# Kernel tuning notes

Hardware: AMD Instinct MI355X
Metric: run time of the kernel (lower is better)

The kernel has to match this reference:

```python
import jax, jax.numpy as jnp
import numpy as np

B, N, DIM, HEADS, DH, EDGE, DEPTH, K = 4, 128, 256, 8, 64, 64, 2, 512
INNER = HEADS * DH
SCALE = DH ** -0.5


def _ln(x, g, b, eps=1e-5):
    m = x.mean(-1, keepdims=True)
    v = ((x - m) ** 2).mean(-1, keepdims=True)
    return (x - m) / jnp.sqrt(v + eps) * g + b


def _rotate_half(x):
    # interleaved pairs: (d r) with r=2 -> (-x2, x1)
    xp = x.reshape(x.shape[:-1] + (-1, 2))
    x1, x2 = xp[..., 0], xp[..., 1]
    return jnp.stack((-x2, x1), axis=-1).reshape(x.shape)


def _gated_res(x, res, gw):
    gate = jax.nn.sigmoid(jnp.concatenate((x, res, x - res), axis=-1) @ gw)
    return x * gate + res * (1 - gate)


def forward(nodes, edges, edge_ln_g, edge_ln_b, ln1_g, ln1_b, w_exp, b_exp,
            w_q, b_q, w_kv, b_kv, w_ekv, b_ekv, w_out, b_out, gate1_w,
            ln2_g, ln2_b, w_ff1, b_ff1, w_ff2, b_ff2, gate2_w, codebook):
    b, n = nodes.shape[:2]
    # LayerNorm edges over channel dim: (B,C,N,N) -> (B,N,N,C)
    e = _ln(jnp.transpose(edges, (0, 2, 3, 1)), edge_ln_g, edge_ln_b)
    # rotary frequencies over positions, repeated pairwise -> (1, N, DH)
    inv = 1.0 / (10000.0 ** (jnp.arange(0, DH, 2, dtype=jnp.float32) / DH))
    fr = jnp.repeat(jnp.arange(n, dtype=jnp.float32)[:, None] * inv[None, :], 2, axis=-1)
    cos, sin = jnp.cos(fr)[None], jnp.sin(fr)[None]

    def heads3(t):  # (B,N,H*D) -> (B*H,N,D)
        return t.reshape(b, n, HEADS, DH).transpose(0, 2, 1, 3).reshape(b * HEADS, n, DH)

    for i in range(DEPTH):
        # PreNorm + edge-conditioned attention
        x = _ln(nodes, ln1_g[i], ln1_b[i])
        x = x @ w_exp[i] + b_exp[i]
        q = x @ w_q[i] + b_q[i]
        k, v = jnp.split(x @ w_kv[i] + b_kv[i], 2, axis=-1)
        ekv = e @ w_ekv[i] + b_ekv[i]  # (B,N,N,INNER)
        q, k, v = heads3(q), heads3(k), heads3(v)
        ekv = ekv.reshape(b, n, n, HEADS, DH).transpose(0, 3, 1, 2, 4).reshape(b * HEADS, n, n, DH)
        q = q * cos + _rotate_half(q) * sin
        k = k * cos + _rotate_half(k) * sin
        kk = k[:, None, :, :] + ekv  # (BH, i, j, d)
        vv = v[:, None, :, :] + ekv
        sim = jnp.einsum('bid,bijd->bij', q, kk) * SCALE
        att = jax.nn.softmax(sim, axis=-1)
        out = jnp.einsum('bij,bijd->bid', att, vv)
        out = out.reshape(b, HEADS, n, DH).transpose(0, 2, 1, 3).reshape(b, n, INNER)
        out = out @ w_out[i] + b_out[i]
        nodes = _gated_res(out, nodes, gate1_w[i])
        # PreNorm + FeedForward
        h = _ln(nodes, ln2_g[i], ln2_b[i])
        h = jax.nn.gelu(h @ w_ff1[i] + b_ff1[i], approximate=False) @ w_ff2[i] + b_ff2[i]
        nodes = _gated_res(h, nodes, gate2_w[i])

    # VQ codebook nearest-neighbor lookup with straight-through estimator
    z = nodes.reshape(-1, DIM)
    d = (z * z).sum(-1, keepdims=True) - 2.0 * z @ codebook.T + (codebook * codebook).sum(-1)[None, :]
    idx = jnp.argmin(d, axis=-1)
    zq = codebook[idx].reshape(b, n, DIM)
    return nodes + jax.lax.stop_gradient(zq - nodes)


def setup_inputs() -> dict:
    key = jax.random.key(0)
    ks = jax.random.split(key, 16)
    s = 0.02
    inp = {
        'nodes': jax.random.normal(ks[0], (B, N, DIM), jnp.float32),
        'edges': jax.random.normal(ks[1], (B, EDGE, N, N), jnp.float32),
        'edge_ln_g': jnp.ones((EDGE,), jnp.float32),
        'edge_ln_b': jnp.zeros((EDGE,), jnp.float32),
        'ln1_g': jnp.ones((DEPTH, DIM), jnp.float32),
        'ln1_b': jnp.zeros((DEPTH, DIM), jnp.float32),
        'w_exp': s * jax.random.normal(ks[2], (DEPTH, DIM, INNER), jnp.float32),
        'b_exp': jnp.zeros((DEPTH, INNER), jnp.float32),
        'w_q': s * jax.random.normal(ks[3], (DEPTH, INNER, INNER), jnp.float32),
        'b_q': jnp.zeros((DEPTH, INNER), jnp.float32),
        'w_kv': s * jax.random.normal(ks[4], (DEPTH, INNER, 2 * INNER), jnp.float32),
        'b_kv': jnp.zeros((DEPTH, 2 * INNER), jnp.float32),
        'w_ekv': s * jax.random.normal(ks[5], (DEPTH, EDGE, INNER), jnp.float32),
        'b_ekv': jnp.zeros((DEPTH, INNER), jnp.float32),
        'w_out': s * jax.random.normal(ks[6], (DEPTH, INNER, DIM), jnp.float32),
        'b_out': jnp.zeros((DEPTH, DIM), jnp.float32),
        'gate1_w': s * jax.random.normal(ks[7], (DEPTH, 3 * DIM, 1), jnp.float32),
        'ln2_g': jnp.ones((DEPTH, DIM), jnp.float32),
        'ln2_b': jnp.zeros((DEPTH, DIM), jnp.float32),
        'w_ff1': s * jax.random.normal(ks[8], (DEPTH, DIM, 4 * DIM), jnp.float32),
        'b_ff1': jnp.zeros((DEPTH, 4 * DIM), jnp.float32),
        'w_ff2': s * jax.random.normal(ks[9], (DEPTH, 4 * DIM, DIM), jnp.float32),
        'b_ff2': jnp.zeros((DEPTH, DIM), jnp.float32),
        'gate2_w': s * jax.random.normal(ks[10], (DEPTH, 3 * DIM, 1), jnp.float32),
        'codebook': jax.random.uniform(ks[11], (K, DIM), jnp.float32, -1.0 / K, 1.0 / K),
    }
    return inp


def reference(nodes, edges, edge_ln_g, edge_ln_b, ln1_g, ln1_b, w_exp, b_exp,
              w_q, b_q, w_kv, b_kv, w_ekv, b_ekv, w_out, b_out, gate1_w,
              ln2_g, ln2_b, w_ff1, b_ff1, w_ff2, b_ff2, gate2_w, codebook):
    return forward(nodes, edges, edge_ln_g, edge_ln_b, ln1_g, ln1_b, w_exp, b_exp,
                   w_q, b_q, w_kv, b_kv, w_ekv, b_ekv, w_out, b_out, gate1_w,
                   ln2_g, ln2_b, w_ff1, b_ff1, w_ff2, b_ff2, gate2_w, codebook)
```

## Files before the change

kernel.cpp:

```cpp
#include <hip/hip_runtime.h>
#include <math.h>


#define DEV __device__ __forceinline__

constexpr int Bn = 4, Nn = 128, DIMn = 256, HEADSn = 8, DHn = 64, EDGEn = 64,
              DEPTHn = 2, Kn = 512, INNERn = 512;
constexpr int QKVW = 1536;
constexpr int PART = 131072;

DEV float wave_reduce_sum(float v) {
#pragma unroll
  for (int m = 32; m >= 1; m >>= 1) v += __shfl_xor(v, m);
  return v;
}

DEV float block_reduce_sum_256(float v, float* red) {
  v = wave_reduce_sum(v);
  int tid = threadIdx.x;
  if ((tid & 63) == 0) red[tid >> 6] = v;
  __syncthreads();
  v = red[0] + red[1] + red[2] + red[3];
  __syncthreads();
  return v;
}

DEV float gelu_exact(float x) {
  return 0.5f * x * (1.f + erff(x * 0.70710678118654752f));
}

__global__ __launch_bounds__(256) void prep_kernel(
    const float* __restrict__ edges, const float* __restrict__ eg,
    const float* __restrict__ eb, float* __restrict__ e,
    float* __restrict__ eT, float* __restrict__ cost, float* __restrict__ sint,
    const float* __restrict__ nodes_in, const float* __restrict__ ln1_g,
    const float* __restrict__ ln1_b, float* __restrict__ xln,
    float* __restrict__ nodes, const float* __restrict__ wek,
    const float* __restrict__ w_out, const float* __restrict__ bek,
    const float* __restrict__ b_out, float* __restrict__ W2,
    float* __restrict__ b_out2, const float* __restrict__ w_exp,
    const float* __restrict__ b_exp, const float* __restrict__ w_q,
    const float* __restrict__ b_q, const float* __restrict__ w_kv,
    const float* __restrict__ b_kv, float* __restrict__ WqkvF,
    float* __restrict__ bqkvF) {
  __shared__ __align__(16) float smem[4736];
  int blk = blockIdx.x;
  int tid = threadIdx.x;

  if (blk < 12) {
    int t = blk;
    int l = t / 6, seg = t % 6;
    int n = seg * 256 + tid;
    const float* W;
    int ldw;
    float acc;
    if (n < 512) {
      W = w_q + (size_t)l * 512 * 512 + n;
      ldw = 512;
      acc = b_q[l * 512 + n];
    } else {
      W = w_kv + (size_t)l * 512 * 1024 + (n - 512);
      ldw = 1024;
      acc = b_kv[l * 1024 + (n - 512)];
    }
    const float* be = b_exp + l * 512;
#pragma unroll 8
    for (int k = 0; k < 512; ++k) acc += be[k] * W[(size_t)k * ldw];
    bqkvF[l * 1536 + n] = acc;
  } else if (blk < 396) {
    int t = blk - 12;
    int l = t / 192, r = t % 192;
    int by = r / 24, bx = r % 24;
    float* As = smem;
    float* Bs = smem + 32 * 34;
    int n0 = bx * 64;
    const float* Aab = w_exp + (size_t)l * 256 * 512 + (size_t)(by * 32) * 512;
    const float* Wb;
    int ldw;
    if (n0 < 512) {
      Wb = w_q + (size_t)l * 512 * 512 + n0;
      ldw = 512;
    } else {
      Wb = w_kv + (size_t)l * 512 * 1024 + (n0 - 512);
      ldw = 1024;
    }
    int arow = tid >> 3, acol = (tid & 7) << 2;
    int brow = tid >> 4, bcol = (tid & 15) << 2;
    int tx = tid & 15, ty = tid >> 4;
    float4 a_nxt = *(const float4*)(Aab + (size_t)arow * 512 + acol);
    float4 b0_nxt = *(const float4*)(Wb + (size_t)brow * ldw + bcol);
    float4 b1_nxt = *(const float4*)(Wb + (size_t)(brow + 16) * ldw + bcol);
    float acc[2][4] = {};
    for (int k0 = 0; k0 < 512; k0 += 32) {
      As[(acol + 0) * 34 + arow] = a_nxt.x;
      As[(acol + 1) * 34 + arow] = a_nxt.y;
      As[(acol + 2) * 34 + arow] = a_nxt.z;
      As[(acol + 3) * 34 + arow] = a_nxt.w;
      *(float4*)&Bs[brow * 68 + bcol] = b0_nxt;
      *(float4*)&Bs[(brow + 16) * 68 + bcol] = b1_nxt;
      __syncthreads();
      int kn = k0 + 32;
      if (kn < 512) {
        a_nxt = *(const float4*)(Aab + (size_t)arow * 512 + kn + acol);
        b0_nxt = *(const float4*)(Wb + (size_t)(kn + brow) * ldw + bcol);
        b1_nxt = *(const float4*)(Wb + (size_t)(kn + brow + 16) * ldw + bcol);
      }
#pragma unroll
      for (int kk = 0; kk < 32; ++kk) {
        float2 av = *(const float2*)&As[kk * 34 + ty * 2];
        float4 bv = *(const float4*)&Bs[kk * 68 + tx * 4];
        acc[0][0] += av.x * bv.x;
        acc[0][1] += av.x * bv.y;
        acc[0][2] += av.x * bv.z;
        acc[0][3] += av.x * bv.w;
        acc[1][0] += av.y * bv.x;
        acc[1][1] += av.y * bv.y;
        acc[1][2] += av.y * bv.z;
        acc[1][3] += av.y * bv.w;
      }
      __syncthreads();
    }
#pragma unroll
    for (int u = 0; u < 2; ++u) {
      int d = by * 32 + ty * 2 + u;
      float4 o = {acc[u][0], acc[u][1], acc[u][2], acc[u][3]};
      *(float4*)(WqkvF + (size_t)l * 256 * 1536 + (size_t)d * 1536 + n0 +
                 tx * 4) = o;
    }
  } else if (blk < 908) {
    float* ets = smem;
    float* redS = smem + 4224;
    float* redQ = smem + 4480;
    int eidx = blk - 396;
    int i = eidx & 127, b = eidx >> 7;
    int j = tid & 127, half = tid >> 7;
    const float* src = edges + (size_t)b * EDGEn * Nn * Nn +
                       (size_t)(half * 32) * (Nn * Nn) + i * Nn + j;
    float vals[32];
    float s = 0.f, q = 0.f;
#pragma unroll
    for (int cc = 0; cc < 32; ++cc) {
      float x = src[(size_t)cc * (Nn * Nn)];
      vals[cc] = x;
      s += x;
      q += x * x;
    }
    redS[tid] = s;
    redQ[tid] = q;
    __syncthreads();
    float ts = redS[j] + redS[j + 128];
    float tq = redQ[j] + redQ[j + 128];
    float m = ts * (1.0f / 64.0f);
    float var = tq * (1.0f / 64.0f) - m * m;
    float inv = 1.f / sqrtf(var + 1e-5f);
    float* dst = e + ((size_t)(b * Nn + i) * EDGEn) * Nn + j;
#pragma unroll
    for (int cc = 0; cc < 32; ++cc) {
      int c = half * 32 + cc;
      float o = (vals[cc] - m) * inv * eg[c] + eb[c];
      vals[cc] = o;
      dst[(size_t)c * Nn] = o;
    }
    float* dstT = eT + ((size_t)(b * Nn + i) * Nn) * EDGEn;
#pragma unroll
    for (int ch = 0; ch < 2; ++ch) {
      __syncthreads();
      if (half == ch) {
#pragma unroll
        for (int cc = 0; cc < 32; ++cc) ets[j * 33 + cc] = vals[cc];
      }
      __syncthreads();
#pragma unroll
      for (int it = 0; it < 4; ++it) {
        int f4 = it * 256 + tid;
        int jj = f4 >> 3, c4 = (f4 & 7) << 2;
        float4 o4 = {ets[jj * 33 + c4], ets[jj * 33 + c4 + 1],
                     ets[jj * 33 + c4 + 2], ets[jj * 33 + c4 + 3]};
        *(float4*)(dstT + (size_t)jj * EDGEn + ch * 32 + c4) = o4;
      }
    }
  } else if (blk < 972) {
    int t = blk - 908;
    int l = t >> 5, h = (t >> 2) & 7, nt = t & 3;
    float* As = smem;
    float* Bs = smem + 2304;
    const float* wekl = wek + (size_t)l * 64 * 512 + h * 64;
    const float* woutl =
        w_out + (size_t)l * 512 * 256 + (size_t)(h * 64) * 256 + nt * 64;
    int tx = tid & 15, ty = tid >> 4;
    float acc[4][4] = {};
    for (int d0 = 0; d0 < 64; d0 += 32) {
      for (int f = tid; f < 512; f += 256) {
        int c = f >> 3, d4 = (f & 7) << 2;
        *(float4*)&As[c * 36 + d4] =
            *(const float4*)(wekl + (size_t)c * 512 + d0 + d4);
      }
      for (int f = tid; f < 512; f += 256) {
        int dd = f >> 4, n4 = (f & 15) << 2;
        *(float4*)&Bs[dd * 68 + n4] =
            *(const float4*)(woutl + (size_t)(d0 + dd) * 256 + n4);
      }
      __syncthreads();
#pragma unroll
      for (int dd = 0; dd < 32; ++dd) {
        float4 bv = *(const float4*)&Bs[dd * 68 + tx * 4];
#pragma unroll
        for (int u = 0; u < 4; ++u) {
          float a = As[(ty * 4 + u) * 36 + dd];
          acc[u][0] += a * bv.x;
          acc[u][1] += a * bv.y;
          acc[u][2] += a * bv.z;
          acc[u][3] += a * bv.w;
        }
      }
      __syncthreads();
    }
#pragma unroll
    for (int u = 0; u < 4; ++u) {
      float4 o = {acc[u][0], acc[u][1], acc[u][2], acc[u][3]};
      *(float4*)(W2 + (size_t)l * 512 * 256 +
                 (size_t)(h * 64 + ty * 4 + u) * 256 + nt * 64 + tx * 4) = o;
    }
  } else if (blk < 980) {
    int t = blk - 972;
    int l = t >> 2, nt = t & 3;
    float* part = smem;
    int nn = tid & 63, kq = tid >> 6;
    const float* wcol = w_out + (size_t)l * 512 * 256 + nt * 64 + nn;
    float acc = 0.f;
    for (int k = kq * 128; k < kq * 128 + 128; ++k)
      acc += bek[l * 512 + k] * wcol[(size_t)k * 256];
    part[tid] = acc;
    __syncthreads();
    if (tid < 64)
      b_out2[l * 256 + nt * 64 + nn] =
          b_out[l * 256 + nt * 64 + nn] + part[nn] + part[64 + nn] +
          part[128 + nn] + part[192 + nn];
  } else if (blk < 996) {
    int t = (blk - 980) * 256 + tid;
    if (t < Nn * 32) {
      int n = t >> 5, p = t & 31;
      float inv = powf(10000.f, -(float)(2 * p) / 64.f);
      float fr = (float)n * inv;
      cost[t] = cosf(fr);
      sint[t] = sinf(fr);
    }
  } else {
    float* red = smem;
    int row = blk - 996;
    float v = nodes_in[(size_t)row * DIMn + tid];
    nodes[(size_t)row * DIMn + tid] = v;
    float m = block_reduce_sum_256(v, red) * (1.0f / 256.0f);
    float d = v - m;
    float var = block_reduce_sum_256(d * d, red) * (1.0f / 256.0f);
    float inv = 1.f / sqrtf(var + 1e-5f);
    xln[(size_t)row * DIMn + tid] = d * inv * ln1_g[tid] + ln1_b[tid];
  }
}

__global__ __launch_bounds__(256) void gemm_kernel(
    const float* __restrict__ A, const float* __restrict__ A2, int aact,
    const float* __restrict__ W1, int N1, const float* __restrict__ b1,
    const float* __restrict__ W2n, int N2, const float* __restrict__ b2,
    const float* __restrict__ Wkb, int Ksplit, float* __restrict__ C, int M,
    int Ntot, int K, int kspan, int act, const float* __restrict__ cost,
    const float* __restrict__ sint, float* __restrict__ kT) {
  __shared__ float As[32][34];
  __shared__ __align__(16) float Bs[32][68];
  int tid = threadIdx.x;
  int bx = blockIdx.x, by = blockIdx.y, zid = blockIdx.z;
  int tx = tid & 15, ty = tid >> 4;
  int arow = tid >> 3, acol = (tid & 7) << 2;
  int brow = tid >> 4, bcol = (tid & 15) << 2;
  int col0 = bx * 64;
  const float* W = W1;
  const float* bias = b1;
  int Nw = N1, wcol = col0;
  if (W2n && col0 >= N1) {
    W = W2n;
    bias = b2;
    Nw = N2;
    wcol = col0 - N1;
  }
  int kb = zid * kspan, kend = kb + kspan;
  const float* arp = A + (size_t)(by * 32 + arow) * K;
  const float* arp2 = A2 ? A2 + (size_t)(by * 32 + arow) * K : nullptr;

  auto load_a = [&](int kpos) -> float4 {
    float4 a = *(const float4*)(arp + kpos + acol);
    if (arp2) {
      float4 a2 = *(const float4*)(arp2 + kpos + acol);
      a.x += a2.x;
      a.y += a2.y;
      a.z += a2.z;
      a.w += a2.w;
    }
    if (aact == 1) {
      a.x = gelu_exact(a.x);
      a.y = gelu_exact(a.y);
      a.z = gelu_exact(a.z);
      a.w = gelu_exact(a.w);
    }
    return a;
  };

  float4 a_nxt = load_a(kb);
  const float* w0p;
  const float* w1p;
  {
    int kr0 = kb + brow, kr1 = kb + brow + 16;
    w0p = (Ksplit && kr0 >= Ksplit)
              ? Wkb + (size_t)(kr0 - Ksplit) * Nw + wcol + bcol
              : W + (size_t)kr0 * Nw + wcol + bcol;
    w1p = (Ksplit && kr1 >= Ksplit)
              ? Wkb + (size_t)(kr1 - Ksplit) * Nw + wcol + bcol
              : W + (size_t)kr1 * Nw + wcol + bcol;
  }
  float4 b0_nxt = *(const float4*)w0p;
  float4 b1_nxt = *(const float4*)w1p;

  float acc[2][4] = {};
  for (int k0 = kb; k0 < kend; k0 += 32) {
    As[acol + 0][arow] = a_nxt.x;
    As[acol + 1][arow] = a_nxt.y;
    As[acol + 2][arow] = a_nxt.z;
    As[acol + 3][arow] = a_nxt.w;
    *(float4*)&Bs[brow][bcol] = b0_nxt;
    *(float4*)&Bs[brow + 16][bcol] = b1_nxt;
    __syncthreads();
    int kn = k0 + 32;
    if (kn < kend) {
      a_nxt = load_a(kn);
      int kr0 = kn + brow, kr1 = kn + brow + 16;
      w0p = (Ksplit && kr0 >= Ksplit)
                ? Wkb + (size_t)(kr0 - Ksplit) * Nw + wcol + bcol
                : W + (size_t)kr0 * Nw + wcol + bcol;
      w1p = (Ksplit && kr1 >= Ksplit)
                ? Wkb + (size_t)(kr1 - Ksplit) * Nw + wcol + bcol
                : W + (size_t)kr1 * Nw + wcol + bcol;
      b0_nxt = *(const float4*)w0p;
      b1_nxt = *(const float4*)w1p;
    }
#pragma unroll
    for (int kk = 0; kk < 32; ++kk) {
      float2 av = *(const float2*)&As[kk][ty * 2];
      float4 bv = *(const float4*)&Bs[kk][tx * 4];
      acc[0][0] += av.x * bv.x;
      acc[0][1] += av.x * bv.y;
      acc[0][2] += av.x * bv.z;
      acc[0][3] += av.x * bv.w;
      acc[1][0] += av.y * bv.x;
      acc[1][1] += av.y * bv.y;
      acc[1][2] += av.y * bv.z;
      acc[1][3] += av.y * bv.w;
    }
    __syncthreads();
  }
  int ccol = wcol + tx * 4;
  bool ksec = (act == 4) && (col0 >= 512) && (col0 < 1024);
  float* trans = (float*)Bs;
  float* Cz = C + (size_t)zid * M * Ntot;
#pragma unroll
  for (int u = 0; u < 2; ++u) {
    int r = by * 32 + ty * 2 + u;
    float o[4];
#pragma unroll
    for (int w = 0; w < 4; ++w)
      o[w] = acc[u][w] + (zid == 0 ? bias[ccol + w] : 0.f);
    if (act == 1) {
#pragma unroll
      for (int w = 0; w < 4; ++w) o[w] = gelu_exact(o[w]);
    } else if (act == 4 && col0 < 1024) {
      int n = r & 127;
      int p0 = (ccol & 63) >> 1;
      float c0 = cost[n * 32 + p0], s0 = sint[n * 32 + p0];
      float c1 = cost[n * 32 + p0 + 1], s1 = sint[n * 32 + p0 + 1];
      float x0 = o[0], x1 = o[1], x2 = o[2], x3 = o[3];
      o[0] = x0 * c0 - x1 * s0;
      o[1] = x1 * c0 + x0 * s0;
      o[2] = x2 * c1 - x3 * s1;
      o[3] = x3 * c1 + x2 * s1;
    }
    if (ksec) {
#pragma unroll
      for (int w = 0; w < 4; ++w) trans[(tx * 4 + w) * 33 + ty * 2 + u] = o[w];
    } else {
      float4 o4 = {o[0], o[1], o[2], o[3]};
      *(float4*)(Cz + (size_t)r * Ntot + col0 + tx * 4) = o4;
    }
  }
  if (ksec) {
    __syncthreads();
    int h = (col0 - 512) >> 6;
    int bb = (by * 32) >> 7;
#pragma unroll
    for (int q = 0; q < 2; ++q) {
      int f4 = tid * 2 + q;
      int dl = f4 >> 3, j4 = (f4 & 7) << 2;
      int jj = (by * 32 + j4) & 127;
      float4 o4 = {trans[dl * 33 + j4], trans[dl * 33 + j4 + 1],
                   trans[dl * 33 + j4 + 2], trans[dl * 33 + j4 + 3]};
      *(float4*)(kT + ((size_t)(bb * 8 + h) * 64 + dl) * 128 + jj) = o4;
    }
  }
}

__global__ __launch_bounds__(128) void attn_kernel(
    const float* __restrict__ qkv, const float* __restrict__ e,
    const float* __restrict__ eT, const float* __restrict__ kT,
    const float* __restrict__ wek, const float* __restrict__ w_out,
    const float* __restrict__ W2, float* __restrict__ proj) {
  __shared__ __align__(16) float qs[256];
  __shared__ __align__(16) float qes[256];
  __shared__ __align__(16) float att[512];
  __shared__ float avh[512];
  __shared__ float aeh[512];
  __shared__ float wekh[64 * 65];
  int blk = blockIdx.x;
  int iq = blk & 31;
  int bh = blk >> 5;
  int h = bh & 7, b = bh >> 3;
  int i0 = iq * 4;
  int row0 = b * 128 + i0;
  int tid = threadIdx.x;

  for (int f = tid; f < 256; f += 128) {
    int ii = f >> 6, d = f & 63;
    qs[f] = qkv[(size_t)(row0 + ii) * QKVW + h * 64 + d];
  }
  for (int f = tid; f < 4096; f += 128) {
    int c = f >> 6, d = f & 63;
    wekh[c * 65 + d] = wek[(size_t)c * INNERn + h * 64 + d];
  }
  __syncthreads();

  for (int f = tid; f < 256; f += 128) {
    int ii = f >> 6, c = f & 63;
    float acc = 0.f;
#pragma unroll
    for (int d = 0; d < 64; ++d) acc += qs[ii * 64 + d] * wekh[c * 65 + d];
    qes[f] = acc;
  }
  __syncthreads();

  int i2 = tid >> 5, j4 = tid & 31;
  float s0 = 0.f, s1 = 0.f, s2 = 0.f, s3 = 0.f;
  {
    const float* ktb = kT + ((size_t)bh * 64) * 128 + j4 * 4;
#pragma unroll
    for (int d4 = 0; d4 < 64; d4 += 4) {
      float4 q4 = *(const float4*)&qs[i2 * 64 + d4];
      float4 k0 = *(const float4*)(ktb + (size_t)(d4 + 0) * 128);
      float4 k1 = *(const float4*)(ktb + (size_t)(d4 + 1) * 128);
      float4 k2 = *(const float4*)(ktb + (size_t)(d4 + 2) * 128);
      float4 k3 = *(const float4*)(ktb + (size_t)(d4 + 3) * 128);
      s0 += q4.x * k0.x + q4.y * k1.x + q4.z * k2.x + q4.w * k3.x;
      s1 += q4.x * k0.y + q4.y * k1.y + q4.z * k2.y + q4.w * k3.y;
      s2 += q4.x * k0.z + q4.y * k1.z + q4.z * k2.z + q4.w * k3.z;
      s3 += q4.x * k0.w + q4.y * k1.w + q4.z * k2.w + q4.w * k3.w;
    }
    const float* eb = e + ((size_t)(row0 + i2) * 64) * 128 + j4 * 4;
#pragma unroll
    for (int c4 = 0; c4 < 64; c4 += 4) {
      float4 qe4 = *(const float4*)&qes[i2 * 64 + c4];
      float4 e0 = *(const float4*)(eb + (size_t)(c4 + 0) * 128);
      float4 e1 = *(const float4*)(eb + (size_t)(c4 + 1) * 128);
      float4 e2 = *(const float4*)(eb + (size_t)(c4 + 2) * 128);
      float4 e3 = *(const float4*)(eb + (size_t)(c4 + 3) * 128);
      s0 += qe4.x * e0.x + qe4.y * e1.x + qe4.z * e2.x + qe4.w * e3.x;
      s1 += qe4.x * e0.y + qe4.y * e1.y + qe4.z * e2.y + qe4.w * e3.y;
      s2 += qe4.x * e0.z + qe4.y * e1.z + qe4.z * e2.z + qe4.w * e3.z;
      s3 += qe4.x * e0.w + qe4.y * e1.w + qe4.z * e2.w + qe4.w * e3.w;
    }
    s0 *= 0.125f;
    s1 *= 0.125f;
    s2 *= 0.125f;
    s3 *= 0.125f;
  }
  {
    float mx = fmaxf(fmaxf(s0, s1), fmaxf(s2, s3));
#pragma unroll
    for (int m = 16; m >= 1; m >>= 1) mx = fmaxf(mx, __shfl_xor(mx, m));
    float p0 = expf(s0 - mx), p1 = expf(s1 - mx), p2 = expf(s2 - mx),
          p3 = expf(s3 - mx);
    float sm = p0 + p1 + p2 + p3;
#pragma unroll
    for (int m = 16; m >= 1; m >>= 1) sm += __shfl_xor(sm, m);
    float inv = 1.f / sm;
    float4 a4 = {p0 * inv, p1 * inv, p2 * inv, p3 * inv};
    *(float4*)&att[i2 * 128 + j4 * 4] = a4;
  }
  __syncthreads();

  {
    int d = tid & 63, half = tid >> 6;
    float av0 = 0.f, av1 = 0.f, av2 = 0.f, av3 = 0.f;
    float ae0 = 0.f, ae1 = 0.f, ae2 = 0.f, ae3 = 0.f;
    const float* vb = qkv + (size_t)(b * 128) * QKVW + 1024 + h * 64 + d;
    const float* etb = eT + ((size_t)row0 * 128) * 64 + d;
    for (int jq = 0; jq < 16; ++jq) {
      int jb = half * 64 + jq * 4;
      float4 a0 = *(const float4*)&att[0 * 128 + jb];
      float4 a1 = *(const float4*)&att[1 * 128 + jb];
      float4 a2 = *(const float4*)&att[2 * 128 + jb];
      float4 a3 = *(const float4*)&att[3 * 128 + jb];
#pragma unroll
      for (int t = 0; t < 4; ++t) {
        int j = jb + t;
        float vv = vb[(size_t)j * QKVW];
        float at0 = ((const float*)&a0)[t];
        float at1 = ((const float*)&a1)[t];
        float at2 = ((const float*)&a2)[t];
        float at3 = ((const float*)&a3)[t];
        av0 += at0 * vv;
        av1 += at1 * vv;
        av2 += at2 * vv;
        av3 += at3 * vv;
        float e0 = etb[(size_t)j * 64];
        float e1 = etb[8192 + (size_t)j * 64];
        float e2 = etb[16384 + (size_t)j * 64];
        float e3 = etb[24576 + (size_t)j * 64];
        ae0 += at0 * e0;
        ae1 += at1 * e1;
        ae2 += at2 * e2;
        ae3 += at3 * e3;
      }
    }
    avh[half * 256 + 0 * 64 + d] = av0;
    avh[half * 256 + 1 * 64 + d] = av1;
    avh[half * 256 + 2 * 64 + d] = av2;
    avh[half * 256 + 3 * 64 + d] = av3;
    aeh[half * 256 + 0 * 64 + d] = ae0;
    aeh[half * 256 + 1 * 64 + d] = ae1;
    aeh[half * 256 + 2 * 64 + d] = ae2;
    aeh[half * 256 + 3 * 64 + d] = ae3;
  }
  __syncthreads();

  for (int f = tid; f < 256; f += 128) {
    int ii = f >> 6, dd = f & 63;
    att[ii * 128 + dd] = avh[ii * 64 + dd] + avh[256 + ii * 64 + dd];
    att[ii * 128 + 64 + dd] = aeh[ii * 64 + dd] + aeh[256 + ii * 64 + dd];
  }
  __syncthreads();

  {
    int rp = tid >> 6, n4 = (tid & 63) << 2;
    int r0 = rp * 2, r1 = rp * 2 + 1;
    float o0[4] = {}, o1[4] = {};
    const float* wo = w_out + (size_t)(h * 64) * 256 + n4;
#pragma unroll 8
    for (int k = 0; k < 64; ++k) {
      float4 w4 = *(const float4*)(wo + (size_t)k * 256);
      float a0 = att[r0 * 128 + k];
      float a1 = att[r1 * 128 + k];
      o0[0] += a0 * w4.x;
      o0[1] += a0 * w4.y;
      o0[2] += a0 * w4.z;
      o0[3] += a0 * w4.w;
      o1[0] += a1 * w4.x;
      o1[1] += a1 * w4.y;
      o1[2] += a1 * w4.z;
      o1[3] += a1 * w4.w;
    }
    const float* w2 = W2 + (size_t)(h * 64) * 256 + n4;
#pragma unroll 8
    for (int k = 0; k < 64; ++k) {
      float4 w4 = *(const float4*)(w2 + (size_t)k * 256);
      float a0 = att[r0 * 128 + 64 + k];
      float a1 = att[r1 * 128 + 64 + k];
      o0[0] += a0 * w4.x;
      o0[1] += a0 * w4.y;
      o0[2] += a0 * w4.z;
      o0[3] += a0 * w4.w;
      o1[0] += a1 * w4.x;
      o1[1] += a1 * w4.y;
      o1[2] += a1 * w4.z;
      o1[3] += a1 * w4.w;
    }
    float* pp = proj + (size_t)h * PART;
    float4 v0 = {o0[0], o0[1], o0[2], o0[3]};
    float4 v1 = {o1[0], o1[1], o1[2], o1[3]};
    *(float4*)(pp + (size_t)(row0 + r0) * 256 + n4) = v0;
    *(float4*)(pp + (size_t)(row0 + r1) * 256 + n4) = v1;
  }
}

__global__ __launch_bounds__(256) void gate_ln_kernel(
    const float* __restrict__ x, int nparts, const float* __restrict__ badd,
    float* __restrict__ nodes, const float* __restrict__ gw,
    const float* __restrict__ lng, const float* __restrict__ lnb,
    float* __restrict__ xln) {
  __shared__ float red[4];
  int row = blockIdx.x, tid = threadIdx.x;
  size_t off = (size_t)row * DIMn + tid;
  float xv = x[off];
  for (int p = 1; p < nparts; ++p) xv += x[off + (size_t)p * PART];
  if (badd) xv += badd[tid];
  float rv = nodes[off];
  float pv =
      xv * gw[tid] + rv * gw[DIMn + tid] + (xv - rv) * gw[2 * DIMn + tid];
  float ssum = block_reduce_sum_256(pv, red);
  float gsig = 1.f / (1.f + expf(-ssum));
  float nv = xv * gsig + rv * (1.f - gsig);
  nodes[off] = nv;
  if (lng) {
    float m = block_reduce_sum_256(nv, red) * (1.0f / 256.0f);
    float d = nv - m;
    float var = block_reduce_sum_256(d * d, red) * (1.0f / 256.0f);
    float inv = 1.f / sqrtf(var + 1e-5f);
    xln[off] = d * inv * lng[tid] + lnb[tid];
  }
}

__global__ __launch_bounds__(256) void vq_kernel(
    const float* __restrict__ nodes, const float* __restrict__ codebook,
    float* __restrict__ out) {
  __shared__ __align__(16) float zs[4 * 256];
  __shared__ float wval[4][4];
  __shared__ int widx[4][4];
  __shared__ int fidx[4];
  int row0 = blockIdx.x * 4;
  int tid = threadIdx.x;
  for (int f = tid; f < 1024; f += 256) zs[f] = nodes[(size_t)row0 * DIMn + f];
  __syncthreads();
  int k1 = tid, k2 = tid + 256;
  const float4* c1p = (const float4*)(codebook + (size_t)k1 * DIMn);
  const float4* c2p = (const float4*)(codebook + (size_t)k2 * DIMn);
  float dot[4][2] = {};
  float cc0 = 0.f, cc1 = 0.f;
#pragma unroll 8
  for (int d4 = 0; d4 < 64; ++d4) {
    float4 c1 = c1p[d4], c2 = c2p[d4];
    cc0 += c1.x * c1.x + c1.y * c1.y + c1.z * c1.z + c1.w * c1.w;
    cc1 += c2.x * c2.x + c2.y * c2.y + c2.z * c2.z + c2.w * c2.w;
#pragma unroll
    for (int r = 0; r < 4; ++r) {
      float4 z = *(const float4*)&zs[r * 256 + d4 * 4];
      dot[r][0] += c1.x * z.x + c1.y * z.y + c1.z * z.z + c1.w * z.w;
      dot[r][1] += c2.x * z.x + c2.y * z.y + c2.z * z.z + c2.w * z.w;
    }
  }
  int lane = tid & 63, w = tid >> 6;
#pragma unroll
  for (int r = 0; r < 4; ++r) {
    float bv = cc0 - 2.f * dot[r][0];
    int bi = k1;
    float v2 = cc1 - 2.f * dot[r][1];
    if (v2 < bv) {
      bv = v2;
      bi = k2;
    }
#pragma unroll
    for (int m = 32; m >= 1; m >>= 1) {
      float ov = __shfl_xor(bv, m);
      int oi = __shfl_xor(bi, m);
      if (ov < bv || (ov == bv && oi < bi)) {
        bv = ov;
        bi = oi;
      }
    }
    if (lane == 0) {
      wval[r][w] = bv;
      widx[r][w] = bi;
    }
  }
  __syncthreads();
  if (tid < 4) {
    float bb = wval[tid][0];
    int bi = widx[tid][0];
    for (int t = 1; t < 4; ++t)
      if (wval[tid][t] < bb || (wval[tid][t] == bb && widx[tid][t] < bi)) {
        bb = wval[tid][t];
        bi = widx[tid][t];
      }
    fidx[tid] = bi;
  }
  __syncthreads();
  for (int f = tid; f < 1024; f += 256) {
    int r = f >> 8, d = f & 255;
    float zv = zs[f];
    float zq = codebook[(size_t)fidx[r] * DIMn + d];
    out[(size_t)(row0 + r) * DIMn + d] = zv + (zq - zv);
  }
}

extern "C" void kernel_launch(void* const* d_in, const int* in_sizes, int n_in,
                              void* d_out, int out_size, void* d_ws,
                              size_t ws_size, hipStream_t stream) {
  const float* nodes_in = (const float*)d_in[0];
  const float* edges = (const float*)d_in[1];
  const float* edge_ln_g = (const float*)d_in[2];
  const float* edge_ln_b = (const float*)d_in[3];
  const float* ln1_g = (const float*)d_in[4];
  const float* ln1_b = (const float*)d_in[5];
  const float* w_exp = (const float*)d_in[6];
  const float* b_exp = (const float*)d_in[7];
  const float* w_q = (const float*)d_in[8];
  const float* b_q = (const float*)d_in[9];
  const float* w_kv = (const float*)d_in[10];
  const float* b_kv = (const float*)d_in[11];
  const float* w_ekv = (const float*)d_in[12];
  const float* b_ekv = (const float*)d_in[13];
  const float* w_out = (const float*)d_in[14];
  const float* b_out = (const float*)d_in[15];
  const float* gate1_w = (const float*)d_in[16];
  const float* ln2_g = (const float*)d_in[17];
  const float* ln2_b = (const float*)d_in[18];
  const float* w_ff1 = (const float*)d_in[19];
  const float* b_ff1 = (const float*)d_in[20];
  const float* w_ff2 = (const float*)d_in[21];
  const float* b_ff2 = (const float*)d_in[22];
  const float* gate2_w = (const float*)d_in[23];
  const float* codebook = (const float*)d_in[24];

  float* ws = (float*)d_ws;
  float* e_buf = ws;
  float* eT_buf = e_buf + 4194304;
  float* cost = eT_buf + 4194304;
  float* sint = cost + 4096;
  float* nodes = sint + 4096;
  float* xln = nodes + 131072;
  float* qkvb = xln + 131072;
  float* kTb = qkvb + 786432;
  float* proj = kTb + 262144;
  float* ff1 = proj + 1048576;
  float* W2buf = ff1 + 1048576;
  float* bout2 = W2buf + 262144;
  float* WqkvF = bout2 + 512;
  float* bqkvF = WqkvF + 786432;

  prep_kernel<<<1508, 256, 0, stream>>>(
      edges, edge_ln_g, edge_ln_b, e_buf, eT_buf, cost, sint, nodes_in, ln1_g,
      ln1_b, xln, nodes, w_ekv, w_out, b_ekv, b_out, W2buf, bout2, w_exp,
      b_exp, w_q, b_q, w_kv, b_kv, WqkvF, bqkvF);

  for (int l = 0; l < DEPTHn; ++l) {
    gemm_kernel<<<dim3(24, 16, 1), 256, 0, stream>>>(
        xln, nullptr, 0, WqkvF + (size_t)l * 256 * 1536, 1536,
        bqkvF + l * 1536, nullptr, 0, nullptr, nullptr, 0, qkvb, 512, QKVW,
        256, 256, 4, cost, sint, kTb);
    attn_kernel<<<1024, 128, 0, stream>>>(qkvb, e_buf, eT_buf, kTb,
                                          w_ekv + l * 64 * 512,
                                          w_out + l * 512 * 256,
                                          W2buf + l * 512 * 256, proj);
    gate_ln_kernel<<<512, 256, 0, stream>>>(
        proj, 8, bout2 + l * 256, nodes, gate1_w + l * 768, ln2_g + l * 256,
        ln2_b + l * 256, xln);
    gemm_kernel<<<dim3(16, 16, 2), 256, 0, stream>>>(
        xln, nullptr, 0, w_ff1 + l * 256 * 1024, 1024, b_ff1 + l * 1024,
        nullptr, 0, nullptr, nullptr, 0, ff1, 512, 1024, 256, 128, 0, cost,
        sint, nullptr);
    gemm_kernel<<<dim3(4, 16, 4), 256, 0, stream>>>(
        ff1, ff1 + 524288, 1, w_ff2 + l * 1024 * 256, 256, b_ff2 + l * 256,
        nullptr, 0, nullptr, nullptr, 0, proj, 512, 256, 1024, 256, 0, cost,
        sint, nullptr);
    const float* nlng = (l + 1 < DEPTHn) ? ln1_g + (l + 1) * 256 : nullptr;
    const float* nlnb = (l + 1 < DEPTHn) ? ln1_b + (l + 1) * 256 : nullptr;
    gate_ln_kernel<<<512, 256, 0, stream>>>(proj, 4, nullptr, nodes,
                                            gate2_w + l * 768, nlng, nlnb,
                                            xln);
  }
  vq_kernel<<<128, 256, 0, stream>>>(nodes, codebook, (float*)d_out);
}
```

Measured before the change: 317.9 us.

## Fuse gated-residual LayerNorm into attention and FF2 via last-block counters

Removes the two standalone gate_ln launches per layer. Each row group keeps an atomic counter, and the last block to finish runs the gated residual, the reduction over the partial sums and the LayerNorm. The counters are zeroed in an extra prep block and reset by that last block. This cuts four launches and their global round trips. In exchange it adds threadfence and atomic overhead, and the tail work runs serially inside one block per row group.

After: 495.6 us. +55.9%, slower.

```diff
diff --git a/kernel.cpp b/kernel.cpp
--- a/kernel.cpp
+++ b/kernel.cpp
@@ -42,7 +42,7 @@
     const float* __restrict__ b_exp, const float* __restrict__ w_q,
     const float* __restrict__ b_q, const float* __restrict__ w_kv,
     const float* __restrict__ b_kv, float* __restrict__ WqkvF,
-    float* __restrict__ bqkvF) {
+    float* __restrict__ bqkvF, int* __restrict__ gcnt) {
   __shared__ __align__(16) float smem[4736];
   int blk = blockIdx.x;
   int tid = threadIdx.x;
@@ -245,7 +245,7 @@
       cost[t] = cosf(fr);
       sint[t] = sinf(fr);
     }
-  } else {
+  } else if (blk < 1508) {
     float* red = smem;
     int row = blk - 996;
     float v = nodes_in[(size_t)row * DIMn + tid];
@@ -255,6 +255,8 @@
     float var = block_reduce_sum_256(d * d, red) * (1.0f / 256.0f);
     float inv = 1.f / sqrtf(var + 1e-5f);
     xln[(size_t)row * DIMn + tid] = d * inv * ln1_g[tid] + ln1_b[tid];
+  } else {
+    if (tid < 160) gcnt[tid] = 0;
   }
 }
 
@@ -405,17 +407,157 @@
   }
 }
 
+__global__ __launch_bounds__(256) void gemm_ff2_kernel(
+    const float* __restrict__ A, const float* __restrict__ A2,
+    const float* __restrict__ W1, const float* __restrict__ b1,
+    float* __restrict__ C, int M, int Ntot, int K, int kspan,
+    int* __restrict__ gcnt, const float* __restrict__ gw,
+    const float* __restrict__ lng, const float* __restrict__ lnb,
+    float* __restrict__ nodes, float* __restrict__ xln) {
+  __shared__ float As[32][34];
+  __shared__ __align__(16) float Bs[32][68];
+  __shared__ int lastf;
+  int tid = threadIdx.x;
+  int bx = blockIdx.x, by = blockIdx.y, zid = blockIdx.z;
+  int tx = tid & 15, ty = tid >> 4;
+  int arow = tid >> 3, acol = (tid & 7) << 2;
+  int brow = tid >> 4, bcol = (tid & 15) << 2;
+  int col0 = bx * 64;
+  int kb = zid * kspan, kend = kb + kspan;
+  const float* arp = A + (size_t)(by * 32 + arow) * K;
+  const float* arp2 = A2 + (size_t)(by * 32 + arow) * K;
+
+  auto load_a = [&](int kpos) -> float4 {
+    float4 a = *(const float4*)(arp + kpos + acol);
+    float4 a2 = *(const float4*)(arp2 + kpos + acol);
+    a.x = gelu_exact(a.x + a2.x);
+    a.y = gelu_exact(a.y + a2.y);
+    a.z = gelu_exact(a.z + a2.z);
+    a.w = gelu_exact(a.w + a2.w);
+    return a;
+  };
+
+  float4 a_nxt = load_a(kb);
+  float4 b0_nxt = *(const float4*)(W1 + (size_t)(kb + brow) * Ntot + col0 + bcol);
+  float4 b1_nxt =
+      *(const float4*)(W1 + (size_t)(kb + brow + 16) * Ntot + col0 + bcol);
+
+  float acc[2][4] = {};
+  for (int k0 = kb; k0 < kend; k0 += 32) {
+    As[acol + 0][arow] = a_nxt.x;
+    As[acol + 1][arow] = a_nxt.y;
+    As[acol + 2][arow] = a_nxt.z;
+    As[acol + 3][arow] = a_nxt.w;
+    *(float4*)&Bs[brow][bcol] = b0_nxt;
+    *(float4*)&Bs[brow + 16][bcol] = b1_nxt;
+    __syncthreads();
+    int kn = k0 + 32;
+    if (kn < kend) {
+      a_nxt = load_a(kn);
+      b0_nxt = *(const float4*)(W1 + (size_t)(kn + brow) * Ntot + col0 + bcol);
+      b1_nxt =
+          *(const float4*)(W1 + (size_t)(kn + brow + 16) * Ntot + col0 + bcol);
+    }
+#pragma unroll
+    for (int kk = 0; kk < 32; ++kk) {
+      float2 av = *(const float2*)&As[kk][ty * 2];
+      float4 bv = *(const float4*)&Bs[kk][tx * 4];
+      acc[0][0] += av.x * bv.x;
+      acc[0][1] += av.x * bv.y;
+      acc[0][2] += av.x * bv.z;
+      acc[0][3] += av.x * bv.w;
+      acc[1][0] += av.y * bv.x;
+      acc[1][1] += av.y * bv.y;
+      acc[1][2] += av.y * bv.z;
+      acc[1][3] += av.y * bv.w;
+    }
+    __syncthreads();
+  }
+  int ccol = col0 + tx * 4;
+  float* Cz = C + (size_t)zid * M * Ntot;
+#pragma unroll
+  for (int u = 0; u < 2; ++u) {
+    int r = by * 32 + ty * 2 + u;
+    float o[4];
+#pragma unroll
+    for (int w = 0; w < 4; ++w)
+      o[w] = acc[u][w] + (zid == 0 ? b1[ccol + w] : 0.f);
+    float4 o4 = {o[0], o[1], o[2], o[3]};
+    *(float4*)(Cz + (size_t)r * Ntot + ccol) = o4;
+  }
+
+  __threadfence();
+  __syncthreads();
+  if (tid == 0) {
+    int old = atomicAdd(gcnt + by, 1);
+    if (old == 15) {
+      gcnt[by] = 0;
+      lastf = 1;
+    } else {
+      lastf = 0;
+    }
+  }
+  __syncthreads();
+  if (!lastf) return;
+  __threadfence();
+  int wv = tid >> 6, lane = tid & 63;
+  for (int rr = 0; rr < 8; ++rr) {
+    int row = by * 32 + wv * 8 + rr;
+    float xv[4], rv[4], nvv[4];
+    float pv = 0.f;
+#pragma unroll
+    for (int cq = 0; cq < 4; ++cq) {
+      int c = lane + cq * 64;
+      float x = C[(size_t)row * 256 + c];
+#pragma unroll
+      for (int p = 1; p < 4; ++p) x += C[(size_t)p * PART + (size_t)row * 256 + c];
+      float rvv = nodes[(size_t)row * 256 + c];
+      xv[cq] = x;
+      rv[cq] = rvv;
+      pv += x * gw[c] + rvv * gw[256 + c] + (x - rvv) * gw[512 + c];
+    }
+    float ssum = wave_reduce_sum(pv);
+    float gsig = 1.f / (1.f + expf(-ssum));
+    float nsum = 0.f;
+#pragma unroll
+    for (int cq = 0; cq < 4; ++cq) {
+      nvv[cq] = xv[cq] * gsig + rv[cq] * (1.f - gsig);
+      nsum += nvv[cq];
+    }
+    float m = wave_reduce_sum(nsum) * (1.0f / 256.0f);
+    float vsum = 0.f;
+#pragma unroll
+    for (int cq = 0; cq < 4; ++cq) {
+      float d = nvv[cq] - m;
+      vsum += d * d;
+    }
+    float var = wave_reduce_sum(vsum) * (1.0f / 256.0f);
+    float inv = 1.f / sqrtf(var + 1e-5f);
+#pragma unroll
+    for (int cq = 0; cq < 4; ++cq) {
+      int c = lane + cq * 64;
+      nodes[(size_t)row * 256 + c] = nvv[cq];
+      if (lng) xln[(size_t)row * 256 + c] = (nvv[cq] - m) * inv * lng[c] + lnb[c];
+    }
+  }
+}
+
 __global__ __launch_bounds__(128) void attn_kernel(
     const float* __restrict__ qkv, const float* __restrict__ e,
     const float* __restrict__ eT, const float* __restrict__ kT,
     const float* __restrict__ wek, const float* __restrict__ w_out,
-    const float* __restrict__ W2, float* __restrict__ proj) {
+    const float* __restrict__ W2, float* __restrict__ proj,
+    int* __restrict__ gcnt, float* __restrict__ nodes,
+    float* __restrict__ xln, const float* __restrict__ gw,
+    const float* __restrict__ lng, const float* __restrict__ lnb,
+    const float* __restrict__ badd) {
   __shared__ __align__(16) float qs[256];
   __shared__ __align__(16) float qes[256];
   __shared__ __align__(16) float att[512];
   __shared__ float avh[512];
   __shared__ float aeh[512];
   __shared__ float wekh[64 * 65];
+  __shared__ int lastf;
   int blk = blockIdx.x;
   int iq = blk & 31;
   int bh = blk >> 5;
@@ -584,32 +726,61 @@
     *(float4*)(pp + (size_t)(row0 + r0) * 256 + n4) = v0;
     *(float4*)(pp + (size_t)(row0 + r1) * 256 + n4) = v1;
   }
-}
-
-__global__ __launch_bounds__(256) void gate_ln_kernel(
-    const float* __restrict__ x, int nparts, const float* __restrict__ badd,
-    float* __restrict__ nodes, const float* __restrict__ gw,
-    const float* __restrict__ lng, const float* __restrict__ lnb,
-    float* __restrict__ xln) {
-  __shared__ float red[4];
-  int row = blockIdx.x, tid = threadIdx.x;
-  size_t off = (size_t)row * DIMn + tid;
-  float xv = x[off];
-  for (int p = 1; p < nparts; ++p) xv += x[off + (size_t)p * PART];
-  if (badd) xv += badd[tid];
-  float rv = nodes[off];
-  float pv =
-      xv * gw[tid] + rv * gw[DIMn + tid] + (xv - rv) * gw[2 * DIMn + tid];
-  float ssum = block_reduce_sum_256(pv, red);
-  float gsig = 1.f / (1.f + expf(-ssum));
-  float nv = xv * gsig + rv * (1.f - gsig);
-  nodes[off] = nv;
-  if (lng) {
-    float m = block_reduce_sum_256(nv, red) * (1.0f / 256.0f);
-    float d = nv - m;
-    float var = block_reduce_sum_256(d * d, red) * (1.0f / 256.0f);
+
+  __threadfence();
+  __syncthreads();
+  if (tid == 0) {
+    int old = atomicAdd(gcnt + (b * 32 + iq), 1);
+    if (old == 7) {
+      gcnt[b * 32 + iq] = 0;
+      lastf = 1;
+    } else {
+      lastf = 0;
+    }
+  }
+  __syncthreads();
+  if (!lastf) return;
+  __threadfence();
+  int wv = tid >> 6, lane = tid & 63;
+  for (int rr = 0; rr < 2; ++rr) {
+    int row = row0 + wv * 2 + rr;
+    float xv[4], rv[4], nvv[4];
+    float pv = 0.f;
+#pragma unroll
+    for (int cq = 0; cq < 4; ++cq) {
+      int c = lane + cq * 64;
+      float x = badd[c];
+#pragma unroll
+      for (int p = 0; p < 8; ++p)
+        x += proj[(size_t)p * PART + (size_t)row * 256 + c];
+      float rvv = nodes[(size_t)row * 256 + c];
+      xv[cq] = x;
+      rv[cq] = rvv;
+      pv += x * gw[c] + rvv * gw[256 + c] + (x - rvv) * gw[512 + c];
+    }
+    float ssum = wave_reduce_sum(pv);
+    float gsig = 1.f / (1.f + expf(-ssum));
+    float nsum = 0.f;
+#pragma unroll
+    for (int cq = 0; cq < 4; ++cq) {
+      nvv[cq] = xv[cq] * gsig + rv[cq] * (1.f - gsig);
+      nsum += nvv[cq];
+    }
+    float m = wave_reduce_sum(nsum) * (1.0f / 256.0f);
+    float vsum = 0.f;
+#pragma unroll
+    for (int cq = 0; cq < 4; ++cq) {
+      float d = nvv[cq] - m;
+      vsum += d * d;
+    }
+    float var = wave_reduce_sum(vsum) * (1.0f / 256.0f);
     float inv = 1.f / sqrtf(var + 1e-5f);
-    xln[off] = d * inv * lng[tid] + lnb[tid];
+#pragma unroll
+    for (int cq = 0; cq < 4; ++cq) {
+      int c = lane + cq * 64;
+      nodes[(size_t)row * 256 + c] = nvv[cq];
+      xln[(size_t)row * 256 + c] = (nvv[cq] - m) * inv * lng[c] + lnb[c];
+    }
   }
 }
 
@@ -729,37 +900,32 @@
   float* bout2 = W2buf + 262144;
   float* WqkvF = bout2 + 512;
   float* bqkvF = WqkvF + 786432;
-
-  prep_kernel<<<1508, 256, 0, stream>>>(
+  int* gcnt = (int*)(bqkvF + 3072);
+
+  prep_kernel<<<1509, 256, 0, stream>>>(
       edges, edge_ln_g, edge_ln_b, e_buf, eT_buf, cost, sint, nodes_in, ln1_g,
       ln1_b, xln, nodes, w_ekv, w_out, b_ekv, b_out, W2buf, bout2, w_exp,
-      b_exp, w_q, b_q, w_kv, b_kv, WqkvF, bqkvF);
+      b_exp, w_q, b_q, w_kv, b_kv, WqkvF, bqkvF, gcnt);
 
   for (int l = 0; l < DEPTHn; ++l) {
     gemm_kernel<<<dim3(24, 16, 1), 256, 0, stream>>>(
         xln, nullptr, 0, WqkvF + (size_t)l * 256 * 1536, 1536,
         bqkvF + l * 1536, nullptr, 0, nullptr, nullptr, 0, qkvb, 512, QKVW,
         256, 256, 4, cost, sint, kTb);
-    attn_kernel<<<1024, 128, 0, stream>>>(qkvb, e_buf, eT_buf, kTb,
-                                          w_ekv + l * 64 * 512,
-                                          w_out + l * 512 * 256,
-                                          W2buf + l * 512 * 256, proj);
-    gate_ln_kernel<<<512, 256, 0, stream>>>(
-        proj, 8, bout2 + l * 256, nodes, gate1_w + l * 768, ln2_g + l * 256,
-        ln2_b + l * 256, xln);
+    attn_kernel<<<1024, 128, 0, stream>>>(
+        qkvb, e_buf, eT_buf, kTb, w_ekv + l * 64 * 512, w_out + l * 512 * 256,
+        W2buf + l * 512 * 256, proj, gcnt, nodes, xln, gate1_w + l * 768,
+        ln2_g + l * 256, ln2_b + l * 256, bout2 + l * 256);
     gemm_kernel<<<dim3(16, 16, 2), 256, 0, stream>>>(
         xln, nullptr, 0, w_ff1 + l * 256 * 1024, 1024, b_ff1 + l * 1024,
         nullptr, 0, nullptr, nullptr, 0, ff1, 512, 1024, 256, 128, 0, cost,
         sint, nullptr);
-    gemm_kernel<<<dim3(4, 16, 4), 256, 0, stream>>>(
-        ff1, ff1 + 524288, 1, w_ff2 + l * 1024 * 256, 256, b_ff2 + l * 256,
-        nullptr, 0, nullptr, nullptr, 0, proj, 512, 256, 1024, 256, 0, cost,
-        sint, nullptr);
     const float* nlng = (l + 1 < DEPTHn) ? ln1_g + (l + 1) * 256 : nullptr;
     const float* nlnb = (l + 1 < DEPTHn) ? ln1_b + (l + 1) * 256 : nullptr;
-    gate_ln_kernel<<<512, 256, 0, stream>>>(proj, 4, nullptr, nodes,
-                                            gate2_w + l * 768, nlng, nlnb,
-                                            xln);
+    gemm_ff2_kernel<<<dim3(4, 16, 4), 256, 0, stream>>>(
+        ff1, ff1 + 524288, w_ff2 + l * 1024 * 256, b_ff2 + l * 256, proj, 512,
+        256, 1024, 256, gcnt + 128, gate2_w + l * 768, nlng, nlnb, nodes,
+        xln);
   }
   vq_kernel<<<128, 256, 0, stream>>>(nodes, codebook, (float*)d_out);
 }
```
